# Kernel optimization log

Hardware: AMD Instinct MI355X
Metric: run time of the kernel (lower is better)

Reference implementation:

```python
import jax, jax.numpy as jnp
import numpy as np

TEMPERATURE = 0.02
B, S, D_TOK, H = 128, 32, 128, 128  # batch, query tokens, doc tokens, hidden dim


def setup_inputs() -> dict:
    key = jax.random.key(0)
    kq, kp = jax.random.split(key)
    query_embeddings = jax.random.normal(kq, (B, S, H), dtype=jnp.float32)
    positive_embeddings = jax.random.normal(kp, (B, D_TOK, H), dtype=jnp.float32)
    return {"query_embeddings": query_embeddings, "positive_embeddings": positive_embeddings}


def reference(query_embeddings, positive_embeddings):
    # Late interaction: [b, c, s, d] = every query token vs every doc token (in-batch negatives)
    late = jnp.einsum('bsh,cdh->bcsd', query_embeddings, positive_embeddings)
    # MaxSim over doc tokens, sum over query tokens -> [b, c] score matrix
    scores = late.max(axis=-1).sum(axis=-1) / TEMPERATURE
    # In-batch negatives: label for row i is column i (the diagonal is the positive)
    logp = jax.nn.log_softmax(scores, axis=-1)
    loss = -jnp.mean(jnp.diagonal(logp))
    return loss
```

## Files before the change

### kernel.cpp

```cpp
#include <hip/hip_runtime.h>
#include <hip/hip_bf16.h>

typedef __bf16 bf16x8 __attribute__((ext_vector_type(8)));
typedef __bf16 bf16x4 __attribute__((ext_vector_type(4)));
typedef float  f32x4  __attribute__((ext_vector_type(4)));

#define Q_CHUNKS (128 * 512)
#define WS_NEED  ((size_t)Q_CHUNKS * 16 + 128 * 128 * 4)

__global__ __launch_bounds__(256) void convert_q(
    const float* __restrict__ Q, unsigned short* __restrict__ wq)
{
    const int g = blockIdx.x * 256 + threadIdx.x;
    const int b = g >> 9, j = g & 511;
    const int si = j >> 8, k = (j >> 6) & 3, l = j & 63;
    const float* src = Q + (size_t)b * 4096 + (si * 16 + (l & 15)) * 128 + k * 32 + (l >> 4) * 8;
    float4 v0 = *(const float4*)src;
    float4 v1 = *(const float4*)(src + 4);
    bf16x8 o = { (__bf16)v0.x, (__bf16)v0.y, (__bf16)v0.z, (__bf16)v0.w,
                 (__bf16)v1.x, (__bf16)v1.y, (__bf16)v1.z, (__bf16)v1.w };
    *(bf16x8*)(wq + ((size_t)g << 3)) = o;
}

__global__ __launch_bounds__(256, 2) void colbert_scores_pfold(
    const float* __restrict__ P,
    const unsigned short* __restrict__ Qb,
    float* __restrict__ scores)
{
    __shared__ __align__(16) unsigned short ps[128 * 128];

    const int tid  = threadIdx.x;
    const int lane = tid & 63;
    const int wave = tid >> 6;

    const int xcd = blockIdx.x & 7;
    const int i   = blockIdx.x >> 3;
    const int c   = (xcd << 4) + (i & 15);
    const int qtr = i >> 4;
    const int bbase = (qtr << 5) + (wave << 3);

    {
        const float4* gp = (const float4*)(P + ((size_t)c << 14));
        #pragma unroll
        for (int t = 0; t < 16; t++) {
            const int j = t * 256 + tid;
            float4 v = gp[j];
            const int d = j >> 5, q = j & 31;
            const int frag = ((d >> 4) << 2) + (q >> 3);
            const int l    = (d & 15) + (((q & 7) >> 1) << 4);
            bf16x4 o = { (__bf16)v.x, (__bf16)v.y, (__bf16)v.z, (__bf16)v.w };
            *(bf16x4*)&ps[(frag << 9) + (l << 3) + ((q & 1) << 2)] = o;
        }
    }
    __syncthreads();

    bf16x8 bp[8][4];
    #pragma unroll
    for (int dj = 0; dj < 8; dj++)
        #pragma unroll
        for (int k = 0; k < 4; k++)
            bp[dj][k] = *(const bf16x8*)&ps[(((dj << 2) + k) << 9) + (lane << 3)];

    #pragma unroll
    for (int it = 0; it < 8; it++) {
        const int b = bbase + it;
        const unsigned short* qw = Qb + ((size_t)b << 12);

        bf16x8 aq[2][4];
        #pragma unroll
        for (int k = 0; k < 4; k++) {
            aq[0][k] = *(const bf16x8*)(qw + (k << 9) + (lane << 3));
            aq[1][k] = *(const bf16x8*)(qw + 2048 + (k << 9) + (lane << 3));
        }

        float mm0 = -1e30f, mm1 = -1e30f;
        #pragma unroll
        for (int dj = 0; dj < 8; dj++) {
            f32x4 t0 = (f32x4){0.f, 0.f, 0.f, 0.f};
            f32x4 t1 = (f32x4){0.f, 0.f, 0.f, 0.f};
            #pragma unroll
            for (int k = 0; k < 4; k++) {
                t0 = __builtin_amdgcn_mfma_f32_16x16x32_bf16(bp[dj][k], aq[0][k], t0, 0, 0, 0);
                t1 = __builtin_amdgcn_mfma_f32_16x16x32_bf16(bp[dj][k], aq[1][k], t1, 0, 0, 0);
            }
            #pragma unroll
            for (int r = 0; r < 4; r++) {
                mm0 = fmaxf(mm0, t0[r]);
                mm1 = fmaxf(mm1, t1[r]);
            }
        }

        mm0 = fmaxf(mm0, __shfl_xor(mm0, 16));
        mm0 = fmaxf(mm0, __shfl_xor(mm0, 32));
        mm1 = fmaxf(mm1, __shfl_xor(mm1, 16));
        mm1 = fmaxf(mm1, __shfl_xor(mm1, 32));
        float partial = mm0 + mm1;
        partial += __shfl_xor(partial, 1);
        partial += __shfl_xor(partial, 2);
        partial += __shfl_xor(partial, 4);
        partial += __shfl_xor(partial, 8);
        if (lane == 0) scores[b * 128 + c] = partial * 50.0f;
    }
}

__global__ __launch_bounds__(1024) void colbert_loss_kernel(
    const float* __restrict__ scores, unsigned* __restrict__ out)
{
    __shared__ float wpart[16];
    const int lane = threadIdx.x & 63;
    const int wave = threadIdx.x >> 6;
    float acc = 0.f;
    #pragma unroll
    for (int i = 0; i < 8; i++) {
        const int r = wave + (i << 4);
        const float* row = scores + r * 128;
        float v0 = row[lane], v1 = row[lane + 64];
        float mx = fmaxf(v0, v1);
        mx = fmaxf(mx, __shfl_xor(mx, 1));  mx = fmaxf(mx, __shfl_xor(mx, 2));
        mx = fmaxf(mx, __shfl_xor(mx, 4));  mx = fmaxf(mx, __shfl_xor(mx, 8));
        mx = fmaxf(mx, __shfl_xor(mx, 16)); mx = fmaxf(mx, __shfl_xor(mx, 32));
        float e = expf(v0 - mx) + expf(v1 - mx);
        e += __shfl_xor(e, 1);  e += __shfl_xor(e, 2);  e += __shfl_xor(e, 4);
        e += __shfl_xor(e, 8);  e += __shfl_xor(e, 16); e += __shfl_xor(e, 32);
        float diag = (r < 64) ? __shfl(v0, r) : __shfl(v1, r - 64);
        acc += diag - (mx + logf(e));
    }
    if (lane == 0) wpart[wave] = acc;
    __syncthreads();
    if (threadIdx.x == 0) {
        float t = 0.f;
        #pragma unroll
        for (int i = 0; i < 16; i++) t += wpart[i];
        float loss = -t / 128.0f;
        unsigned bits = __float_as_uint(loss);
        unsigned rnd  = (bits + 0x7FFFu + ((bits >> 16) & 1u)) & 0xFFFF0000u;
        out[0] = rnd | (rnd >> 16);
    }
}

__global__ __launch_bounds__(256, 2) void colbert_scores_slow(
    const float* __restrict__ Q, const float* __restrict__ P, float* __restrict__ scores)
{
    __shared__ __align__(16) unsigned short qs[4 * 32 * 128];
    __shared__ __align__(16) unsigned short ps[128 * 128];
    const int tid = threadIdx.x;
    const int b0 = (blockIdx.x & 31) * 4, c0 = (blockIdx.x >> 5) * 4;
    const float4* gq = (const float4*)(Q + (size_t)b0 * 4096);
    #pragma unroll
    for (int j = tid; j < 4096; j += 256) {
        float4 v = gq[j];
        int f = j << 2, row = f >> 7, h = f & 127;
        int dst = (row << 7) + (((h >> 3) ^ (row & 15)) << 3) + (h & 7);
        bf16x4 o = { (__bf16)v.x, (__bf16)v.y, (__bf16)v.z, (__bf16)v.w };
        *(bf16x4*)&qs[dst] = o;
    }
    const int lane = tid & 63, wave = tid >> 6, n = lane & 15, quad = lane >> 4;
    const unsigned short* qb = qs + wave * 4096;
    #pragma unroll 1
    for (int it = 0; it < 4; it++) {
        const int c = c0 + it;
        if (it) __syncthreads();
        const float4* gp = (const float4*)(P + (size_t)c * 16384);
        #pragma unroll
        for (int j = tid; j < 4096; j += 256) {
            float4 v = gp[j];
            int f = j << 2, d = f >> 7, h = f & 127;
            int dst = (d << 7) + (((h >> 3) ^ (d & 15)) << 3) + (h & 7);
            bf16x4 o = { (__bf16)v.x, (__bf16)v.y, (__bf16)v.z, (__bf16)v.w };
            *(bf16x4*)&ps[dst] = o;
        }
        __syncthreads();
        f32x4 acc[2][8];
        #pragma unroll
        for (int si = 0; si < 2; si++)
            #pragma unroll
            for (int dj = 0; dj < 8; dj++) acc[si][dj] = (f32x4){0.f,0.f,0.f,0.f};
        #pragma unroll
        for (int k = 0; k < 4; k++) {
            const int chunk = (((k << 2) + quad) ^ n) << 3;
            bf16x8 a0 = *(const bf16x8*)&qb[(n << 7) + chunk];
            bf16x8 a1 = *(const bf16x8*)&qb[((n + 16) << 7) + chunk];
            #pragma unroll
            for (int dj = 0; dj < 8; dj++) {
                bf16x8 bb = *(const bf16x8*)&ps[((dj * 16 + n) << 7) + chunk];
                acc[0][dj] = __builtin_amdgcn_mfma_f32_16x16x32_bf16(a0, bb, acc[0][dj], 0, 0, 0);
                acc[1][dj] = __builtin_amdgcn_mfma_f32_16x16x32_bf16(a1, bb, acc[1][dj], 0, 0, 0);
            }
        }
        float partial = 0.f;
        #pragma unroll
        for (int si = 0; si < 2; si++)
            #pragma unroll
            for (int r = 0; r < 4; r++) {
                float m = acc[si][0][r];
                #pragma unroll
                for (int dj = 1; dj < 8; dj++) m = fmaxf(m, acc[si][dj][r]);
                m = fmaxf(m, __shfl_xor(m, 1)); m = fmaxf(m, __shfl_xor(m, 2));
                m = fmaxf(m, __shfl_xor(m, 4)); m = fmaxf(m, __shfl_xor(m, 8));
                partial += m;
            }
        partial += __shfl_xor(partial, 16);
        partial += __shfl_xor(partial, 32);
        if (lane == 0) scores[(b0 + wave) * 128 + c] = partial * 50.0f;
    }
}

extern "C" void kernel_launch(void* const* d_in, const int* in_sizes, int n_in,
                              void* d_out, int out_size, void* d_ws, size_t ws_size,
                              hipStream_t stream) {
    const float* Q = (const float*)d_in[0];
    const float* P = (const float*)d_in[1];

    if (ws_size >= WS_NEED) {
        unsigned short* wq = (unsigned short*)d_ws;
        float* scores = (float*)(wq + (size_t)Q_CHUNKS * 8);
        convert_q<<<dim3(256), dim3(256), 0, stream>>>(Q, wq);
        colbert_scores_pfold<<<dim3(512), dim3(256), 0, stream>>>(P, wq, scores);
        colbert_loss_kernel<<<dim3(1), dim3(1024), 0, stream>>>(scores, (unsigned*)d_out);
    } else {
        float* scores = (float*)d_ws;
        colbert_scores_slow<<<dim3(1024), dim3(256), 0, stream>>>(Q, P, scores);
        colbert_loss_kernel<<<dim3(1), dim3(1024), 0, stream>>>(scores, (unsigned*)d_out);
    }
}
```

Measured before the change: 83.23 us.

## Fuse Q conversion, score GEMM and loss into one cooperative kernel

Replaces the three separate launches (Q bf16 conversion, score computation, log-softmax loss) with a single cooperative kernel that uses grid-wide syncs between phases. This removes two kernel launch gaps at the cost of two grid barriers and a single-block loss tail. The slow fallback path for small workspace is dropped, and the three-kernel path is kept only if the cooperative launch fails.

```diff
diff --git a/kernel.cpp b/kernel.cpp
--- a/kernel.cpp
+++ b/kernel.cpp
@@ -1,5 +1,8 @@
 #include <hip/hip_runtime.h>
 #include <hip/hip_bf16.h>
+#include <hip/hip_cooperative_groups.h>
+
+namespace cg = cooperative_groups;
 
 typedef __bf16 bf16x8 __attribute__((ext_vector_type(8)));
 typedef __bf16 bf16x4 __attribute__((ext_vector_type(4)));
@@ -7,6 +10,146 @@
 
 #define Q_CHUNKS (128 * 512)
 #define WS_NEED  ((size_t)Q_CHUNKS * 16 + 128 * 128 * 4)
+
+__global__ __launch_bounds__(256, 2) void colbert_fused(
+    const float* __restrict__ Q,
+    const float* __restrict__ P,
+    unsigned short* __restrict__ wq,
+    float* __restrict__ scores,
+    unsigned* __restrict__ out)
+{
+    __shared__ __align__(16) unsigned short ps[128 * 128];
+    __shared__ float wpart[4];
+
+    cg::grid_group grid = cg::this_grid();
+
+    const int tid  = threadIdx.x;
+    const int lane = tid & 63;
+    const int wave = tid >> 6;
+
+    {
+        const int t  = blockIdx.x * 256 + tid;
+        const int w4 = t << 2;
+        const int b  = w4 >> 12;
+        const int rem = w4 & 4095;
+        const int si = rem >> 11, k = (rem >> 9) & 3, l = (rem >> 3) & 63, e0 = rem & 7;
+        const float* src = Q + (b << 12) + (si * 16 + (l & 15)) * 128
+                             + (k << 5) + ((l >> 4) << 3) + e0;
+        float4 v = *(const float4*)src;
+        bf16x4 o = { (__bf16)v.x, (__bf16)v.y, (__bf16)v.z, (__bf16)v.w };
+        *(bf16x4*)(wq + w4) = o;
+    }
+    __threadfence();
+    grid.sync();
+
+    const int xcd = blockIdx.x & 7;
+    const int i   = blockIdx.x >> 3;
+    const int c   = (xcd << 4) + (i & 15);
+    const int qtr = i >> 4;
+    const int bbase = (qtr << 5) + (wave << 3);
+
+    {
+        const float4* gp = (const float4*)(P + ((size_t)c << 14));
+        #pragma unroll
+        for (int t = 0; t < 16; t++) {
+            const int j = t * 256 + tid;
+            float4 v = gp[j];
+            const int d = j >> 5, q = j & 31;
+            const int frag = ((d >> 4) << 2) + (q >> 3);
+            const int l    = (d & 15) + (((q & 7) >> 1) << 4);
+            bf16x4 o = { (__bf16)v.x, (__bf16)v.y, (__bf16)v.z, (__bf16)v.w };
+            *(bf16x4*)&ps[(frag << 9) + (l << 3) + ((q & 1) << 2)] = o;
+        }
+    }
+    __syncthreads();
+
+    bf16x8 bp[8][4];
+    #pragma unroll
+    for (int dj = 0; dj < 8; dj++)
+        #pragma unroll
+        for (int k = 0; k < 4; k++)
+            bp[dj][k] = *(const bf16x8*)&ps[(((dj << 2) + k) << 9) + (lane << 3)];
+
+    #pragma unroll
+    for (int it = 0; it < 8; it++) {
+        const int b = bbase + it;
+        const unsigned short* qw = wq + ((size_t)b << 12);
+
+        bf16x8 aq[2][4];
+        #pragma unroll
+        for (int k = 0; k < 4; k++) {
+            aq[0][k] = *(const bf16x8*)(qw + (k << 9) + (lane << 3));
+            aq[1][k] = *(const bf16x8*)(qw + 2048 + (k << 9) + (lane << 3));
+        }
+
+        float mm0 = -1e30f, mm1 = -1e30f;
+        #pragma unroll
+        for (int dj = 0; dj < 8; dj++) {
+            f32x4 t0 = (f32x4){0.f, 0.f, 0.f, 0.f};
+            f32x4 t1 = (f32x4){0.f, 0.f, 0.f, 0.f};
+            #pragma unroll
+            for (int k = 0; k < 4; k++) {
+                t0 = __builtin_amdgcn_mfma_f32_16x16x32_bf16(bp[dj][k], aq[0][k], t0, 0, 0, 0);
+                t1 = __builtin_amdgcn_mfma_f32_16x16x32_bf16(bp[dj][k], aq[1][k], t1, 0, 0, 0);
+            }
+            #pragma unroll
+            for (int r = 0; r < 4; r++) {
+                mm0 = fmaxf(mm0, t0[r]);
+                mm1 = fmaxf(mm1, t1[r]);
+            }
+        }
+
+        mm0 = fmaxf(mm0, __shfl_xor(mm0, 16));
+        mm0 = fmaxf(mm0, __shfl_xor(mm0, 32));
+        mm1 = fmaxf(mm1, __shfl_xor(mm1, 16));
+        mm1 = fmaxf(mm1, __shfl_xor(mm1, 32));
+        float partial = mm0 + mm1;
+        partial += __shfl_xor(partial, 1);
+        partial += __shfl_xor(partial, 2);
+        partial += __shfl_xor(partial, 4);
+        partial += __shfl_xor(partial, 8);
+        if (lane == 0) scores[b * 128 + c] = partial * 50.0f;
+    }
+
+    __threadfence();
+    grid.sync();
+
+    if (blockIdx.x == 0) {
+        float accl = 0.f;
+        #pragma unroll 1
+        for (int g = 0; g < 4; g++) {
+            float a0[8], a1[8];
+            #pragma unroll
+            for (int j = 0; j < 8; j++) {
+                const int r = (wave << 5) + (g << 3) + j;
+                a0[j] = scores[r * 128 + lane];
+                a1[j] = scores[r * 128 + 64 + lane];
+            }
+            #pragma unroll
+            for (int j = 0; j < 8; j++) {
+                const int r = (wave << 5) + (g << 3) + j;
+                float mx = fmaxf(a0[j], a1[j]);
+                mx = fmaxf(mx, __shfl_xor(mx, 1));  mx = fmaxf(mx, __shfl_xor(mx, 2));
+                mx = fmaxf(mx, __shfl_xor(mx, 4));  mx = fmaxf(mx, __shfl_xor(mx, 8));
+                mx = fmaxf(mx, __shfl_xor(mx, 16)); mx = fmaxf(mx, __shfl_xor(mx, 32));
+                float e = expf(a0[j] - mx) + expf(a1[j] - mx);
+                e += __shfl_xor(e, 1);  e += __shfl_xor(e, 2);  e += __shfl_xor(e, 4);
+                e += __shfl_xor(e, 8);  e += __shfl_xor(e, 16); e += __shfl_xor(e, 32);
+                float diag = (r < 64) ? __shfl(a0[j], r) : __shfl(a1[j], r - 64);
+                accl += diag - (mx + logf(e));
+            }
+        }
+        if (lane == 0) wpart[wave] = accl;
+        __syncthreads();
+        if (tid == 0) {
+            float t = wpart[0] + wpart[1] + wpart[2] + wpart[3];
+            float loss = -t / 128.0f;
+            unsigned bits = __float_as_uint(loss);
+            unsigned rnd  = (bits + 0x7FFFu + ((bits >> 16) & 1u)) & 0xFFFF0000u;
+            out[0] = rnd | (rnd >> 16);
+        }
+    }
+}
 
 __global__ __launch_bounds__(256) void convert_q(
     const float* __restrict__ Q, unsigned short* __restrict__ wq)
@@ -28,17 +171,14 @@
     float* __restrict__ scores)
 {
     __shared__ __align__(16) unsigned short ps[128 * 128];
-
     const int tid  = threadIdx.x;
     const int lane = tid & 63;
     const int wave = tid >> 6;
-
     const int xcd = blockIdx.x & 7;
     const int i   = blockIdx.x >> 3;
     const int c   = (xcd << 4) + (i & 15);
     const int qtr = i >> 4;
     const int bbase = (qtr << 5) + (wave << 3);
-
     {
         const float4* gp = (const float4*)(P + ((size_t)c << 14));
         #pragma unroll
@@ -53,26 +193,22 @@
         }
     }
     __syncthreads();
-
     bf16x8 bp[8][4];
     #pragma unroll
     for (int dj = 0; dj < 8; dj++)
         #pragma unroll
         for (int k = 0; k < 4; k++)
             bp[dj][k] = *(const bf16x8*)&ps[(((dj << 2) + k) << 9) + (lane << 3)];
-
     #pragma unroll
     for (int it = 0; it < 8; it++) {
         const int b = bbase + it;
         const unsigned short* qw = Qb + ((size_t)b << 12);
-
         bf16x8 aq[2][4];
         #pragma unroll
         for (int k = 0; k < 4; k++) {
             aq[0][k] = *(const bf16x8*)(qw + (k << 9) + (lane << 3));
             aq[1][k] = *(const bf16x8*)(qw + 2048 + (k << 9) + (lane << 3));
         }
-
         float mm0 = -1e30f, mm1 = -1e30f;
         #pragma unroll
         for (int dj = 0; dj < 8; dj++) {
@@ -89,7 +225,6 @@
                 mm1 = fmaxf(mm1, t1[r]);
             }
         }
-
         mm0 = fmaxf(mm0, __shfl_xor(mm0, 16));
         mm0 = fmaxf(mm0, __shfl_xor(mm0, 32));
         mm1 = fmaxf(mm1, __shfl_xor(mm1, 16));
@@ -138,88 +273,21 @@
     }
 }
 
-__global__ __launch_bounds__(256, 2) void colbert_scores_slow(
-    const float* __restrict__ Q, const float* __restrict__ P, float* __restrict__ scores)
-{
-    __shared__ __align__(16) unsigned short qs[4 * 32 * 128];
-    __shared__ __align__(16) unsigned short ps[128 * 128];
-    const int tid = threadIdx.x;
-    const int b0 = (blockIdx.x & 31) * 4, c0 = (blockIdx.x >> 5) * 4;
-    const float4* gq = (const float4*)(Q + (size_t)b0 * 4096);
-    #pragma unroll
-    for (int j = tid; j < 4096; j += 256) {
-        float4 v = gq[j];
-        int f = j << 2, row = f >> 7, h = f & 127;
-        int dst = (row << 7) + (((h >> 3) ^ (row & 15)) << 3) + (h & 7);
-        bf16x4 o = { (__bf16)v.x, (__bf16)v.y, (__bf16)v.z, (__bf16)v.w };
-        *(bf16x4*)&qs[dst] = o;
-    }
-    const int lane = tid & 63, wave = tid >> 6, n = lane & 15, quad = lane >> 4;
-    const unsigned short* qb = qs + wave * 4096;
-    #pragma unroll 1
-    for (int it = 0; it < 4; it++) {
-        const int c = c0 + it;
-        if (it) __syncthreads();
-        const float4* gp = (const float4*)(P + (size_t)c * 16384);
-        #pragma unroll
-        for (int j = tid; j < 4096; j += 256) {
-            float4 v = gp[j];
-            int f = j << 2, d = f >> 7, h = f & 127;
-            int dst = (d << 7) + (((h >> 3) ^ (d & 15)) << 3) + (h & 7);
-            bf16x4 o = { (__bf16)v.x, (__bf16)v.y, (__bf16)v.z, (__bf16)v.w };
-            *(bf16x4*)&ps[dst] = o;
-        }
-        __syncthreads();
-        f32x4 acc[2][8];
-        #pragma unroll
-        for (int si = 0; si < 2; si++)
-            #pragma unroll
-            for (int dj = 0; dj < 8; dj++) acc[si][dj] = (f32x4){0.f,0.f,0.f,0.f};
-        #pragma unroll
-        for (int k = 0; k < 4; k++) {
-            const int chunk = (((k << 2) + quad) ^ n) << 3;
-            bf16x8 a0 = *(const bf16x8*)&qb[(n << 7) + chunk];
-            bf16x8 a1 = *(const bf16x8*)&qb[((n + 16) << 7) + chunk];
-            #pragma unroll
-            for (int dj = 0; dj < 8; dj++) {
-                bf16x8 bb = *(const bf16x8*)&ps[((dj * 16 + n) << 7) + chunk];
-                acc[0][dj] = __builtin_amdgcn_mfma_f32_16x16x32_bf16(a0, bb, acc[0][dj], 0, 0, 0);
-                acc[1][dj] = __builtin_amdgcn_mfma_f32_16x16x32_bf16(a1, bb, acc[1][dj], 0, 0, 0);
-            }
-        }
-        float partial = 0.f;
-        #pragma unroll
-        for (int si = 0; si < 2; si++)
-            #pragma unroll
-            for (int r = 0; r < 4; r++) {
-                float m = acc[si][0][r];
-                #pragma unroll
-                for (int dj = 1; dj < 8; dj++) m = fmaxf(m, acc[si][dj][r]);
-                m = fmaxf(m, __shfl_xor(m, 1)); m = fmaxf(m, __shfl_xor(m, 2));
-                m = fmaxf(m, __shfl_xor(m, 4)); m = fmaxf(m, __shfl_xor(m, 8));
-                partial += m;
-            }
-        partial += __shfl_xor(partial, 16);
-        partial += __shfl_xor(partial, 32);
-        if (lane == 0) scores[(b0 + wave) * 128 + c] = partial * 50.0f;
-    }
-}
-
 extern "C" void kernel_launch(void* const* d_in, const int* in_sizes, int n_in,
                               void* d_out, int out_size, void* d_ws, size_t ws_size,
                               hipStream_t stream) {
     const float* Q = (const float*)d_in[0];
     const float* P = (const float*)d_in[1];
-
-    if (ws_size >= WS_NEED) {
-        unsigned short* wq = (unsigned short*)d_ws;
-        float* scores = (float*)(wq + (size_t)Q_CHUNKS * 8);
+    unsigned short* wq = (unsigned short*)d_ws;
+    float* scores = (float*)(wq + (size_t)Q_CHUNKS * 8);
+    unsigned* out = (unsigned*)d_out;
+
+    void* args[] = { (void*)&Q, (void*)&P, (void*)&wq, (void*)&scores, (void*)&out };
+    hipError_t err = hipLaunchCooperativeKernel(
+        (const void*)colbert_fused, dim3(512), dim3(256), args, 0, stream);
+    if (err != hipSuccess) {
         convert_q<<<dim3(256), dim3(256), 0, stream>>>(Q, wq);
         colbert_scores_pfold<<<dim3(512), dim3(256), 0, stream>>>(P, wq, scores);
-        colbert_loss_kernel<<<dim3(1), dim3(1024), 0, stream>>>(scores, (unsigned*)d_out);
-    } else {
-        float* scores = (float*)d_ws;
-        colbert_scores_slow<<<dim3(1024), dim3(256), 0, stream>>>(Q, P, scores);
-        colbert_loss_kernel<<<dim3(1), dim3(1024), 0, stream>>>(scores, (unsigned*)d_out);
-    }
-}
+        colbert_loss_kernel<<<dim3(1), dim3(1024), 0, stream>>>(scores, out);
+    }
+}
```

Result: slower. 302.5 us (+263.5%).
